# Performance work log

Hardware: AMD Instinct MI355X
Metric: run time of the kernel (lower is better)

## Reference

```python
import jax, jax.numpy as jnp
import numpy as np

# 5x5 Gaussian-Laplacian template: kernel = (4*GL) * GL_T, with a2=-a1/8, a3=-a1/16
GL_T = np.zeros((5, 5), np.float32)
GL_T[2, 2] = 1.0
for r, c in [(1, 2), (2, 1), (2, 3), (3, 2)]:
    GL_T[r, c] = -1.0 / 8.0
for r, c in [(0, 2), (1, 1), (1, 3), (2, 0), (2, 4), (3, 1), (3, 3), (4, 2)]:
    GL_T[r, c] = -1.0 / 16.0

SOB0 = np.array([[1, 2, 1], [0, 0, 0], [-1, -2, -1]], np.float32)
SOB45 = np.array([[2, 1, 0], [1, 0, -1], [0, -1, -2]], np.float32)
SOB90 = np.array([[1, 0, -1], [2, 0, -2], [1, 0, -1]], np.float32)
SOB135 = np.array([[0, -1, -2], [1, 0, -1], [2, 1, 0]], np.float32)

# cubic-spaced threshold value table: (10-0)*(i/100)^3, i=0..100
X_VALUES = np.array([10.0 * (i / 100.0) ** 3 for i in range(101)], np.float32)


def conv2d(x, w, stride=1, padding=0):
    return jax.lax.conv_general_dilated(
        x, w, (stride, stride), ((padding, padding), (padding, padding)),
        dimension_numbers=("NCHW", "OIHW", "NCHW"))


def avg_pool(x, k, s, p):
    # PyTorch AvgPool2d default count_include_pad=True -> divide by k*k always
    s_ = jax.lax.reduce_window(x, 0.0, jax.lax.add, (1, 1, k, k), (1, 1, s, s),
                               ((0, 0), (0, 0), (p, p), (p, p)))
    return s_ / float(k * k)


def _gdm(x, gdm_weight, conv_w, bn_gamma, bn_beta, bn_mean, bn_var):
    x = avg_pool(x, 3, 2, 1)                                  # [B,3,H/2,W/2]
    image_a = jnp.mean(x, axis=1, keepdims=True)              # [B,1,h,w]
    y = conv2d(x, conv_w, stride=2, padding=3)                # ConvBN(3,5,7,s2)
    y = (y - bn_mean[None, :, None, None]) * jax.lax.rsqrt(bn_var + 1e-5)[None, :, None, None]
    y = y * bn_gamma[None, :, None, None] + bn_beta[None, :, None, None]
    weight_att = jnp.tanh(jnp.mean(y, axis=(2, 3)))           # [B,5]

    a1 = gdm_weight[0, 0] * 4.0
    kgl = (a1 * jnp.asarray(GL_T))[None, None]                # [1,1,5,5]
    x_GL = jnp.abs(conv2d(image_a, kgl, stride=1, padding=2))
    x_GL = jnp.where(x_GL < 1e-6, 0.0, x_GL)                  # abs/threshold; relu is no-op

    b, _, h, w = x_GL.shape
    x_t = x_GL.reshape(b, 1, -1)                              # [B,1,HW]
    x_max = jnp.max(x_t, axis=-1)                             # [B,1]
    pos = x_t > 0
    all_sum = jnp.sum(pos, axis=-1)                           # [B,1]
    xv = jnp.asarray(X_VALUES)[None, :, None]                 # [1,101,1]
    sub_sum = jnp.sum(pos & (x_t <= xv), axis=-1)             # [B,101]
    percentage = sub_sum / all_sum                            # [B,101] float

    params = jnp.stack([0.2 + 0.05 * weight_att[:, 1],
                        0.4 + 0.05 * weight_att[:, 2],
                        0.6 + 0.05 * weight_att[:, 3],
                        0.8 + 0.05 * weight_att[:, 4]])       # [4,B]
    thr_pct = jnp.sort(params, axis=0).T                      # [B,4]
    z = jnp.abs(percentage[:, None, :] - thr_pct[:, :, None]) # [B,4,101]
    closest = jnp.argmin(z, axis=-1)                          # [B,4]
    threshold = jnp.asarray(X_VALUES)[closest]                # [B,4]

    tmin = jnp.concatenate([jnp.zeros_like(x_max), threshold], axis=-1)[:, :, None]  # [B,5,1]
    tmax = jnp.concatenate([threshold, x_max], axis=-1)[:, :, None]                  # [B,5,1]
    mask = ((x_t > tmin) & (x_t <= tmax)).astype(jnp.float32)                        # [B,5,HW]
    m = mask.reshape(b, 5, h, w)

    m = avg_pool(m, 9, 1, 4)
    m = avg_pool(m, 9, 1, 4)
    m = avg_pool(m, 9, 2, 4)                                  # [B,5,h/2,w/2]
    mf = m.reshape(b, 5, -1)
    mn = jnp.min(mf, axis=2, keepdims=True)
    mx = jnp.max(mf, axis=2, keepdims=True)
    return ((mf - mn) / (mx - mn)).reshape(b, 5, h // 2, w // 2)


def _hge(feat, hge_weight, fc_w, fc_b):
    # directional kernels built from entries of the learned 3x3 weight
    Sob0 = hge_weight[:, :, 0, 0][:, :, None, None]
    Sob45 = hge_weight[:, :, 0, 1][:, :, None, None]
    Sob90 = hge_weight[:, :, 0, 2][:, :, None, None]
    Sob135 = hge_weight[:, :, 1, 0][:, :, None, None]
    a1 = (hge_weight[:, :, 2, 2] * 4.0)[:, :, None, None]
    x_0 = conv2d(feat, Sob0 * jnp.asarray(SOB0), 1, 1)
    x_45 = conv2d(feat, Sob45 * jnp.asarray(SOB45), 1, 1)
    x_90 = conv2d(feat, Sob90 * jnp.asarray(SOB90), 1, 1)
    x_135 = conv2d(feat, Sob135 * jnp.asarray(SOB135), 1, 1)
    x_GL = conv2d(feat, a1 * jnp.asarray(GL_T), 1, 2)
    x_out = jnp.concatenate([x_0, x_45, x_90, x_135, x_GL], axis=1)  # [B,5*C,H,W]
    return conv2d(x_out, fc_w) + fc_b[None, :, None, None]


def setup_inputs() -> dict:
    key = jax.random.key(0)
    ks = jax.random.split(key, 6)
    return {
        "x": jax.random.normal(ks[0], (8, 3, 512, 512), jnp.float32),
        "gdm_weight": jax.random.normal(ks[1], (1, 5), jnp.float32) * 0.5,
        "conv_w": jax.random.normal(ks[2], (5, 3, 7, 7), jnp.float32) * 0.05,
        "bn_gamma": jnp.ones((5,), jnp.float32),
        "bn_beta": jnp.zeros((5,), jnp.float32),
        "bn_mean": jnp.zeros((5,), jnp.float32),
        "bn_var": jnp.ones((5,), jnp.float32),
        "feat": jax.random.normal(ks[3], (8, 64, 128, 128), jnp.float32),
        "hge_weight": jax.random.normal(ks[4], (64, 64, 3, 3), jnp.float32) * 0.05,
        "fc_w": jax.random.normal(ks[5], (64, 320, 1, 1), jnp.float32) * 0.05,
        "fc_b": jnp.zeros((64,), jnp.float32),
    }


def reference(x, gdm_weight, conv_w, bn_gamma, bn_beta, bn_mean, bn_var,
              feat, hge_weight, fc_w, fc_b):
    gdm_out = _gdm(x, gdm_weight, conv_w, bn_gamma, bn_beta, bn_mean, bn_var)
    hge_out = _hge(feat, hge_weight, fc_w, fc_b)
    return gdm_out, hge_out
```

## Files before the change

### kernel.cpp

```cpp
#include <hip/hip_runtime.h>
#include <hip/hip_bf16.h>
#include <math.h>

#define WS_AT    0
#define WS_YSUM  20480
#define WS_XMAX  20520
#define WS_HIST  20528
#define WS_MN    21376
#define WS_MX    21440
#define WS_XP    21504
#define WS_IA    1594368
#define WS_XGL   2118656

#define GDM_OUT  655360

static __device__ __forceinline__ float xv_val(int i) {
    double t = (double)i / 100.0;
    return (float)(10.0 * t * t * t);
}

__global__ __launch_bounds__(256) void k_front(const float* __restrict__ x,
                                               const float* __restrict__ hw,
                                               const float* __restrict__ fcw,
                                               float* __restrict__ xp,
                                               float* __restrict__ ia,
                                               float* __restrict__ At,
                                               float* __restrict__ zr,
                                               unsigned* __restrict__ mnb,
                                               unsigned* __restrict__ mxb) {
    int bid = blockIdx.x;
    if (bid < 2048) {
        int idx = bid * 256 + threadIdx.x;
        int b = idx >> 16; int p = idx & 65535; int oy = p >> 8; int ox = p & 255;
        float cs[3];
#pragma unroll
        for (int c = 0; c < 3; ++c) {
            const float* src = x + (((size_t)(b * 3 + c)) << 18);
            float s = 0.f;
#pragma unroll
            for (int dy = -1; dy <= 1; ++dy) {
                int iy = 2 * oy + dy; if ((unsigned)iy >= 512u) continue;
#pragma unroll
                for (int dx = -1; dx <= 1; ++dx) {
                    int ix = 2 * ox + dx; if ((unsigned)ix >= 512u) continue;
                    s += src[iy * 512 + ix];
                }
            }
            cs[c] = s * (1.f / 9.f);
            xp[(((size_t)(b * 3 + c)) << 16) + p] = cs[c];
        }
        ia[(((size_t)b) << 16) + p] = (cs[0] + cs[1] + cs[2]) * (1.f / 3.f);
    } else if (bid < 2128) {
        int idx = (bid - 2048) * 256 + threadIdx.x;
        int o = idx & 63; int k = idx >> 6;
        int d = k >> 6; int c = k & 63;
        const int goff[5] = {0, 1, 2, 3, 8};
        float s = 0.f;
        for (int m = 0; m < 64; ++m)
            s += fcw[o * 320 + d * 64 + m] * hw[(m * 64 + c) * 9 + goff[d]];
        At[k * 64 + o] = s * ((d == 4) ? 4.f : 1.f);
    } else {
#pragma unroll
        for (int q = 0; q < 4; ++q) {
            int i = threadIdx.x + 256 * q;
            if (i < 864) zr[i] = 0.f;
        }
        if (threadIdx.x < 40) mnb[threadIdx.x] = 0x7f7fffffu;
        else if (threadIdx.x < 80) mxb[threadIdx.x - 40] = 0u;
    }
}

__global__ __launch_bounds__(256) void k_convgl(const float* __restrict__ xp,
                                                const float* __restrict__ w,
                                                float* __restrict__ ysum,
                                                const float* __restrict__ ia,
                                                const float* __restrict__ gdmw,
                                                float* __restrict__ xgl,
                                                int* __restrict__ hist,
                                                unsigned* __restrict__ xmax) {
    __shared__ float wsm[735];
    __shared__ float red[256];
    __shared__ float xv[101];
    __shared__ int sh[102];
    int bid = blockIdx.x;
    int tid = threadIdx.x;
    if (bid < 512) {
        int b = bid >> 6;
        int p = (bid & 63) * 256 + tid;
        int oy = p >> 7, ox = p & 127;
        for (int l = tid; l < 735; l += 256) wsm[l] = w[l];
        __syncthreads();
        float s[5] = {0.f, 0.f, 0.f, 0.f, 0.f};
        for (int ic = 0; ic < 3; ++ic) {
            const float* src = xp + (((size_t)(b * 3 + ic)) << 16);
#pragma unroll
            for (int r = 0; r < 7; ++r) {
                int iy = 2 * oy - 3 + r; if ((unsigned)iy >= 256u) continue;
#pragma unroll
                for (int ss = 0; ss < 7; ++ss) {
                    int ix = 2 * ox - 3 + ss; if ((unsigned)ix >= 256u) continue;
                    float v = src[iy * 256 + ix];
                    int wi = (ic * 7 + r) * 7 + ss;
#pragma unroll
                    for (int co = 0; co < 5; ++co) s[co] = fmaf(wsm[co * 147 + wi], v, s[co]);
                }
            }
        }
#pragma unroll
        for (int co = 0; co < 5; ++co) {
            red[tid] = s[co]; __syncthreads();
            for (int off = 128; off > 0; off >>= 1) {
                if (tid < off) red[tid] += red[tid + off];
                __syncthreads();
            }
            if (tid == 0) atomicAdd(&ysum[b * 5 + co], red[0]);
            __syncthreads();
        }
    } else {
        int idx = bid - 512;
        int b = idx >> 8;
        int p = (idx & 255) * 256 + tid;
        int y = p >> 8, x = p & 255;
        if (tid < 101) xv[tid] = xv_val(tid);
        if (tid < 102) sh[tid] = 0;
        __syncthreads();
        const float* src = ia + (((size_t)b) << 16);
        float a1 = gdmw[0] * 4.f;
        auto rd = [&](int dy, int dx) -> float {
            int iy = y + dy, ix = x + dx;
            if ((unsigned)iy >= 256u || (unsigned)ix >= 256u) return 0.f;
            return src[iy * 256 + ix];
        };
        float acc = rd(0, 0)
            - 0.125f  * (rd(-1, 0) + rd(0, -1) + rd(0, 1) + rd(1, 0))
            - 0.0625f * (rd(-2, 0) + rd(-1, -1) + rd(-1, 1) + rd(0, -2) +
                         rd(0, 2) + rd(1, -1) + rd(1, 1) + rd(2, 0));
        float raw = fabsf(a1 * acc);
        float val = (raw < 1e-6f) ? 0.f : raw;
        xgl[(((size_t)b) << 16) + p] = val;
        if (val > 0.f) {
            int lo = 0, hi = 101;
            while (lo < hi) { int mid = (lo + hi) >> 1; if (val <= xv[mid]) hi = mid; else lo = mid + 1; }
            atomicAdd(&sh[lo], 1);
        }
        red[tid] = val; __syncthreads();
        for (int off = 128; off > 0; off >>= 1) {
            if (tid < off) red[tid] = fmaxf(red[tid], red[tid + off]);
            __syncthreads();
        }
        if (tid == 0) atomicMax(&xmax[b], __float_as_uint(red[0]));
        if (tid < 102 && sh[tid]) atomicAdd(&hist[b * 102 + tid], sh[tid]);
    }
}

#define F1_STR 268
__global__ __launch_bounds__(256) void k_hv1(const float* __restrict__ in,
                                             const float* __restrict__ ysum,
                                             const float* __restrict__ gamma,
                                             const float* __restrict__ beta,
                                             const float* __restrict__ mean,
                                             const float* __restrict__ var,
                                             const int* __restrict__ hist,
                                             const unsigned* __restrict__ xmax,
                                             float* __restrict__ outp) {
    int plane = blockIdx.y;
    int r0 = blockIdx.x * 8;
    int b = plane / 5, band = plane - 5 * b;
    __shared__ float sthr[4];
    int tid = threadIdx.x;
    if (tid == 0) {
        float wa[5];
        for (int c = 1; c < 5; ++c) {
            float m = ysum[b * 5 + c] * (1.f / 16384.f);
            wa[c] = tanhf((m - mean[c]) * rsqrtf(var[c] + 1e-5f) * gamma[c] + beta[c]);
        }
        float pr[4] = {0.2f + 0.05f * wa[1], 0.4f + 0.05f * wa[2],
                       0.6f + 0.05f * wa[3], 0.8f + 0.05f * wa[4]};
        auto sw = [&](int i, int j) { if (pr[i] > pr[j]) { float t = pr[i]; pr[i] = pr[j]; pr[j] = t; } };
        sw(0, 1); sw(2, 3); sw(0, 2); sw(1, 3); sw(1, 2);
        int all = 0;
        for (int i = 0; i <= 101; ++i) all += hist[b * 102 + i];
        float bestz[4] = {1e30f, 1e30f, 1e30f, 1e30f};
        int besti[4] = {0, 0, 0, 0};
        int cum = 0;
        for (int i = 0; i <= 100; ++i) {
            cum += hist[b * 102 + i];
            float pct = (float)cum / (float)all;
            for (int t = 0; t < 4; ++t) {
                float z = fabsf(pct - pr[t]);
                if (z < bestz[t]) { bestz[t] = z; besti[t] = i; }
            }
        }
        for (int t = 0; t < 4; ++t) sthr[t] = xv_val(besti[t]);
    }
    __syncthreads();
    float tmin = (band == 0) ? 0.f : sthr[band - 1];
    float tmax = (band == 4) ? __uint_as_float(xmax[b]) : sthr[band];
    const float* src = in + (((size_t)b) << 16);
    __shared__ float mr[16][F1_STR];
    __shared__ float hh[16][256];
    for (int l = tid; l < 16 * 256; l += 256) {
        int i = l >> 8, c = l & 255;
        int rr = r0 - 4 + i;
        float v = ((unsigned)rr < 256u) ? src[rr * 256 + c] : 0.f;
        v = (v > tmin && v <= tmax) ? 1.f : 0.f;
        mr[i][c + 4] = v;
    }
    if (tid < 128) { int i = tid >> 3, p = tid & 7; mr[i][p < 4 ? p : 256 + p] = 0.f; }
    __syncthreads();
    {
        int r = tid >> 4, x0 = (tid & 15) * 16;
        float w[24];
#pragma unroll
        for (int k = 0; k < 6; ++k) {
            float4 q = *(const float4*)&mr[r][x0 + 4 * k];
            w[4 * k] = q.x; w[4 * k + 1] = q.y; w[4 * k + 2] = q.z; w[4 * k + 3] = q.w;
        }
        float o[16];
        float s = 0.f;
#pragma unroll
        for (int k = 0; k < 9; ++k) s += w[k];
#pragma unroll
        for (int j = 0; j < 16; ++j) {
            o[j] = s * (1.f / 9.f);
            if (j < 15) s += w[j + 9] - w[j];
        }
#pragma unroll
        for (int k = 0; k < 4; ++k) {
            float4 q = {o[4 * k], o[4 * k + 1], o[4 * k + 2], o[4 * k + 3]};
            *(float4*)&hh[r][x0 + 4 * k] = q;
        }
    }
    __syncthreads();
    {
        int c = tid;
        float ld[16];
#pragma unroll
        for (int i = 0; i < 16; ++i) ld[i] = hh[i][c];
        float s = 0.f;
#pragma unroll
        for (int k = 0; k < 9; ++k) s += ld[k];
        float* dst = outp + (((size_t)plane) << 16);
#pragma unroll
        for (int j = 0; j < 8; ++j) {
            dst[(r0 + j) * 256 + c] = s * (1.f / 9.f);
            if (j < 7) s += ld[j + 9] - ld[j];
        }
    }
}

__global__ __launch_bounds__(256) void k_hv2s2(const float* __restrict__ in,
                                               float* __restrict__ outp,
                                               unsigned* __restrict__ mnb,
                                               unsigned* __restrict__ mxb) {
    int plane = blockIdx.y;
    int r0 = blockIdx.x * 8;
    __shared__ float mr[31][264];
    __shared__ float hh[31][256];
    int tid = threadIdx.x;
    const float* src = in + (((size_t)plane) << 16);
    for (int l = tid; l < 31 * 264; l += 256) {
        int i = l / 264, c = l - i * 264;
        int rr = 2 * r0 - 8 + i, cc = c - 4;
        mr[i][c] = ((unsigned)rr < 256u && (unsigned)cc < 256u) ? src[rr * 256 + cc] : 0.f;
    }
    __syncthreads();
    for (int l = tid; l < 31 * 256; l += 256) {
        int i = l >> 8, x = l & 255;
        float s = 0.f;
#pragma unroll
        for (int k = 0; k < 9; ++k) s += mr[i][x + k];
        hh[i][x] = s * (1.f / 9.f);
    }
    __syncthreads();
    for (int l = tid; l < 23 * 256; l += 256) {
        int i2 = l >> 8, x = l & 255;
        float s = 0.f;
#pragma unroll
        for (int k = 0; k < 9; ++k) s += hh[i2 + k][x];
        float v = s * (1.f / 9.f);
        if ((unsigned)(2 * r0 - 4 + i2) >= 256u) v = 0.f;
        mr[i2][x + 4] = v;
    }
    if (tid < 184) { int i2 = tid / 8, p = tid & 7; mr[i2][p < 4 ? p : 256 + p] = 0.f; }
    __syncthreads();
    for (int l = tid; l < 23 * 128; l += 256) {
        int i2 = l >> 7, ox = l & 127;
        float s = 0.f;
#pragma unroll
        for (int k = 0; k < 9; ++k) s += mr[i2][2 * ox + k];
        hh[i2][ox] = s * (1.f / 9.f);
    }
    __syncthreads();
    float vmn = 1e30f, vmx = -1e30f;
    float* dst = outp + (size_t)plane * 16384;
#pragma unroll
    for (int q = 0; q < 4; ++q) {
        int l = tid + 256 * q;
        int jj = l >> 7, ox = l & 127;
        float s = 0.f;
#pragma unroll
        for (int k = 0; k < 9; ++k) s += hh[2 * jj + k][ox];
        s *= (1.f / 9.f);
        dst[(r0 + jj) * 128 + ox] = s;
        vmn = fminf(vmn, s); vmx = fmaxf(vmx, s);
    }
    __syncthreads();
    float* smn = &hh[23][0];
    float* smx = &hh[24][0];
    smn[tid] = vmn; smx[tid] = vmx; __syncthreads();
    for (int off = 128; off > 0; off >>= 1) {
        if (tid < off) {
            smn[tid] = fminf(smn[tid], smn[tid + off]);
            smx[tid] = fmaxf(smx[tid], smx[tid + off]);
        }
        __syncthreads();
    }
    if (tid == 0) {
        atomicMin(&mnb[plane], __float_as_uint(smn[0]));
        atomicMax(&mxb[plane], __float_as_uint(smx[0]));
    }
}

__global__ __launch_bounds__(512, 2) void k_hge(const float* __restrict__ feat,
                                                const float* __restrict__ At,
                                                const float* __restrict__ fcb,
                                                const float* __restrict__ p2,
                                                const unsigned* __restrict__ mnb,
                                                const unsigned* __restrict__ mxb,
                                                float* __restrict__ gdm,
                                                float* __restrict__ out) {
    int tile = blockIdx.x, b = blockIdx.y;
    int tid = threadIdx.x;
    if (tile == 64) {
        int base = b * 512 + tid;
#pragma unroll
        for (int q = 0; q < 40; ++q) {
            int i4 = base + 4096 * q;
            int idx = i4 * 4;
            int plane = idx >> 14;
            float mn = __uint_as_float(mnb[plane]), mx = __uint_as_float(mxb[plane]);
            float inv = 1.f / (mx - mn);
            float4 v = *(const float4*)&p2[idx];
            float4 o = {(v.x - mn) * inv, (v.y - mn) * inv, (v.z - mn) * inv, (v.w - mn) * inv};
            *(float4*)&gdm[idx] = o;
        }
        return;
    }
    int ty = (tile >> 3) * 16, tx = (tile & 7) * 16;
    int grp = tid >> 8, tg = tid & 255;
    __shared__ float ft[2][20][21];
    __shared__ float tl[2][5][256];
    __shared__ float al[2][2][5][64];
    int og = tg >> 6;
    int pl = tg & 63;
    float acc[4][8];
#pragma unroll
    for (int i = 0; i < 4; ++i)
#pragma unroll
        for (int j = 0; j < 8; ++j) acc[i][j] = 0.f;

    const float* cur[3];
    int str3[3];
    bool ok[3];
#pragma unroll
    for (int j = 0; j < 3; ++j) {
        int l = tid + 512 * j;
        cur[j] = nullptr; str3[j] = 0; ok[j] = false;
        if (l < 800) {
            int ch = (l >= 400); int rem = l - ch * 400;
            int r = rem / 20, cx = rem - r * 20;
            int gy = ty - 2 + r, gx = tx - 2 + cx;
            if ((unsigned)gy < 128u && (unsigned)gx < 128u) {
                cur[j] = feat + (((size_t)(b * 64 + ch)) << 14) + gy * 128 + gx;
                str3[j] = 2 << 14;
                ok[j] = true;
            }
        } else if (l < 1440) {
            int q = l - 800;
            int ch = (q >= 320); int k = q - ch * 320;
            cur[j] = At + (k >> 6) * 4096 + ch * 64 + (k & 63);
            str3[j] = 128;
            ok[j] = true;
        }
    }
    float pr[3];
#pragma unroll
    for (int j = 0; j < 3; ++j) pr[j] = ok[j] ? *cur[j] : 0.f;

    for (int g = 0; g < 32; ++g) {
        int buf = g & 1;
#pragma unroll
        for (int j = 0; j < 3; ++j) {
            int l = tid + 512 * j;
            if (l < 800) {
                int ch = (l >= 400); int rem = l - ch * 400;
                int r = rem / 20, cx = rem - r * 20;
                ft[ch][r][cx] = pr[j];
            } else if (l < 1440) {
                ((float*)al[buf])[l - 800] = pr[j];
            }
        }
        __syncthreads();
        if (g < 31) {
#pragma unroll
            for (int j = 0; j < 3; ++j) {
                if (ok[j]) { cur[j] += str3[j]; pr[j] = *cur[j]; }
            }
        }
        {
            int cy = (tg >> 4) + 2, cx = (tg & 15) + 2;
            int ch = grp;
            float fm2 = ft[ch][cy - 2][cx], f2p = ft[ch][cy + 2][cx];
            float fl2 = ft[ch][cy][cx - 2], fr2 = ft[ch][cy][cx + 2];
            float a  = ft[ch][cy - 1][cx - 1], bq = ft[ch][cy - 1][cx], cc = ft[ch][cy - 1][cx + 1];
            float dd = ft[ch][cy][cx - 1],     ee = ft[ch][cy][cx],     ffv = ft[ch][cy][cx + 1];
            float g_ = ft[ch][cy + 1][cx - 1], h  = ft[ch][cy + 1][cx], i2 = ft[ch][cy + 1][cx + 1];
            tl[ch][0][tg] = (a + 2.f * bq + cc) - (g_ + 2.f * h + i2);
            tl[ch][1][tg] = 2.f * a + bq + dd - ffv - h - 2.f * i2;
            tl[ch][2][tg] = (a - cc) + 2.f * (dd - ffv) + (g_ - i2);
            tl[ch][3][tg] = -bq - 2.f * cc + dd - ffv + 2.f * g_ + h;
            tl[ch][4][tg] = ee - 0.125f * (bq + dd + ffv + h)
                          - 0.0625f * (fm2 + a + cc + fl2 + fr2 + g_ + i2 + f2p);
        }
        __syncthreads();
#pragma unroll
        for (int ch = 0; ch < 2; ++ch) {
#pragma unroll
            for (int d = 0; d < 5; ++d) {
                float4 a0 = *(const float4*)&al[buf][ch][d][grp * 32 + og * 8];
                float4 a1 = *(const float4*)&al[buf][ch][d][grp * 32 + og * 8 + 4];
                float av[8] = {a0.x, a0.y, a0.z, a0.w, a1.x, a1.y, a1.z, a1.w};
#pragma unroll
                for (int pj = 0; pj < 4; ++pj) {
                    float tv = tl[ch][d][pl + 64 * pj];
#pragma unroll
                    for (int oi = 0; oi < 8; ++oi)
                        acc[pj][oi] = fmaf(av[oi], tv, acc[pj][oi]);
                }
            }
        }
    }
#pragma unroll
    for (int oi = 0; oi < 8; ++oi) {
        int o = grp * 32 + og * 8 + oi;
        float bias = fcb[o];
        float* dsto = out + (((size_t)(b * 64 + o)) << 14);
#pragma unroll
        for (int pj = 0; pj < 4; ++pj) {
            int pxl = pl + 64 * pj;
            dsto[(ty + (pxl >> 4)) * 128 + tx + (pxl & 15)] = acc[pj][oi] + bias;
        }
    }
}

extern "C" void kernel_launch(void* const* d_in, const int* in_sizes, int n_in,
                              void* d_out, int out_size, void* d_ws, size_t ws_size,
                              hipStream_t stream) {
    const float* x    = (const float*)d_in[0];
    const float* gdmw = (const float*)d_in[1];
    const float* convw= (const float*)d_in[2];
    const float* bng  = (const float*)d_in[3];
    const float* bnb  = (const float*)d_in[4];
    const float* bnm  = (const float*)d_in[5];
    const float* bnv  = (const float*)d_in[6];
    const float* feat = (const float*)d_in[7];
    const float* hw   = (const float*)d_in[8];
    const float* fcw  = (const float*)d_in[9];
    const float* fcb  = (const float*)d_in[10];
    float* out = (float*)d_out;
    float* ws  = (float*)d_ws;

    float* At   = ws + WS_AT;
    float* ysum = ws + WS_YSUM;
    unsigned* xmax = (unsigned*)(ws + WS_XMAX);
    int* hist   = (int*)(ws + WS_HIST);
    unsigned* mnb = (unsigned*)(ws + WS_MN);
    unsigned* mxb = (unsigned*)(ws + WS_MX);
    float* xp   = ws + WS_XP;
    float* ia   = ws + WS_IA;
    float* xgl  = ws + WS_XGL;
    float* p2   = ws + WS_XP + 20480;

    float* hge = out + GDM_OUT;
    float* p0  = hge;

    k_front  <<<2129, 256, 0, stream>>>(x, hw, fcw, xp, ia, At, ws + WS_YSUM, mnb, mxb);
    k_convgl <<<2560, 256, 0, stream>>>(xp, convw, ysum, ia, gdmw, xgl, hist, xmax);
    k_hv1    <<<dim3(32, 40), 256, 0, stream>>>(xgl, ysum, bng, bnb, bnm, bnv, hist, xmax, p0);
    k_hv2s2  <<<dim3(16, 40), 256, 0, stream>>>(p0, p2, mnb, mxb);
    k_hge    <<<dim3(65, 8), 512, 0, stream>>>(feat, At, fcb, p2, mnb, mxb, out, hge);
}
```

Before: 251.5 us.

## Fuse band-mask box filter and stride-2 pooling into one kernel

Merges the first 9x9 box filter over the thresholded band mask with the second 9x9 filter and the stride-2 pooling into a single kernel. The intermediate full-resolution plane no longer goes through global memory, and one launch is removed. In exchange each block recomputes a larger halo (39 mask rows), does more shared-memory work, and uses about 74KB of LDS, which may lower occupancy.

```diff
diff --git a/kernel.cpp b/kernel.cpp
--- a/kernel.cpp
+++ b/kernel.cpp
@@ -153,19 +153,22 @@
     }
 }
 
-#define F1_STR 268
-__global__ __launch_bounds__(256) void k_hv1(const float* __restrict__ in,
-                                             const float* __restrict__ ysum,
-                                             const float* __restrict__ gamma,
-                                             const float* __restrict__ beta,
-                                             const float* __restrict__ mean,
-                                             const float* __restrict__ var,
-                                             const int* __restrict__ hist,
-                                             const unsigned* __restrict__ xmax,
-                                             float* __restrict__ outp) {
+__global__ __launch_bounds__(256) void k_pool(const float* __restrict__ xgl,
+                                              const float* __restrict__ ysum,
+                                              const float* __restrict__ gamma,
+                                              const float* __restrict__ beta,
+                                              const float* __restrict__ mean,
+                                              const float* __restrict__ var,
+                                              const int* __restrict__ hist,
+                                              const unsigned* __restrict__ xmax,
+                                              float* __restrict__ p2,
+                                              unsigned* __restrict__ mnb,
+                                              unsigned* __restrict__ mxb) {
     int plane = blockIdx.y;
     int r0 = blockIdx.x * 8;
     int b = plane / 5, band = plane - 5 * b;
+    __shared__ float mk[39][264];
+    __shared__ float p1[31][264];
     __shared__ float sthr[4];
     int tid = threadIdx.x;
     if (tid == 0) {
@@ -174,9 +177,9 @@
             float m = ysum[b * 5 + c] * (1.f / 16384.f);
             wa[c] = tanhf((m - mean[c]) * rsqrtf(var[c] + 1e-5f) * gamma[c] + beta[c]);
         }
-        float pr[4] = {0.2f + 0.05f * wa[1], 0.4f + 0.05f * wa[2],
-                       0.6f + 0.05f * wa[3], 0.8f + 0.05f * wa[4]};
-        auto sw = [&](int i, int j) { if (pr[i] > pr[j]) { float t = pr[i]; pr[i] = pr[j]; pr[j] = t; } };
+        float pr_[4] = {0.2f + 0.05f * wa[1], 0.4f + 0.05f * wa[2],
+                        0.6f + 0.05f * wa[3], 0.8f + 0.05f * wa[4]};
+        auto sw = [&](int i, int j) { if (pr_[i] > pr_[j]) { float t = pr_[i]; pr_[i] = pr_[j]; pr_[j] = t; } };
         sw(0, 1); sw(2, 3); sw(0, 2); sw(1, 3); sw(1, 2);
         int all = 0;
         for (int i = 0; i <= 101; ++i) all += hist[b * 102 + i];
@@ -187,7 +190,7 @@
             cum += hist[b * 102 + i];
             float pct = (float)cum / (float)all;
             for (int t = 0; t < 4; ++t) {
-                float z = fabsf(pct - pr[t]);
+                float z = fabsf(pct - pr_[t]);
                 if (z < bestz[t]) { bestz[t] = z; besti[t] = i; }
             }
         }
@@ -196,118 +199,90 @@
     __syncthreads();
     float tmin = (band == 0) ? 0.f : sthr[band - 1];
     float tmax = (band == 4) ? __uint_as_float(xmax[b]) : sthr[band];
-    const float* src = in + (((size_t)b) << 16);
-    __shared__ float mr[16][F1_STR];
-    __shared__ float hh[16][256];
-    for (int l = tid; l < 16 * 256; l += 256) {
-        int i = l >> 8, c = l & 255;
-        int rr = r0 - 4 + i;
-        float v = ((unsigned)rr < 256u) ? src[rr * 256 + c] : 0.f;
-        v = (v > tmin && v <= tmax) ? 1.f : 0.f;
-        mr[i][c + 4] = v;
-    }
-    if (tid < 128) { int i = tid >> 3, p = tid & 7; mr[i][p < 4 ? p : 256 + p] = 0.f; }
-    __syncthreads();
-    {
-        int r = tid >> 4, x0 = (tid & 15) * 16;
-        float w[24];
-#pragma unroll
-        for (int k = 0; k < 6; ++k) {
-            float4 q = *(const float4*)&mr[r][x0 + 4 * k];
-            w[4 * k] = q.x; w[4 * k + 1] = q.y; w[4 * k + 2] = q.z; w[4 * k + 3] = q.w;
-        }
-        float o[16];
-        float s = 0.f;
-#pragma unroll
-        for (int k = 0; k < 9; ++k) s += w[k];
-#pragma unroll
-        for (int j = 0; j < 16; ++j) {
-            o[j] = s * (1.f / 9.f);
-            if (j < 15) s += w[j + 9] - w[j];
-        }
-#pragma unroll
-        for (int k = 0; k < 4; ++k) {
-            float4 q = {o[4 * k], o[4 * k + 1], o[4 * k + 2], o[4 * k + 3]};
-            *(float4*)&hh[r][x0 + 4 * k] = q;
-        }
+    const float* src = xgl + (((size_t)b) << 16);
+    for (int l = tid; l < 39 * 264; l += 256) {
+        int i = l / 264, c = l - i * 264;
+        int rr = 2 * r0 - 12 + i, cc = c - 4;
+        float m = 0.f;
+        if ((unsigned)rr < 256u && (unsigned)cc < 256u) {
+            float v = src[rr * 256 + cc];
+            m = (v > tmin && v <= tmax) ? 1.f : 0.f;
+        }
+        mk[i][c] = m;
     }
     __syncthreads();
     {
         int c = tid;
-        float ld[16];
-#pragma unroll
-        for (int i = 0; i < 16; ++i) ld[i] = hh[i][c];
-        float s = 0.f;
-#pragma unroll
-        for (int k = 0; k < 9; ++k) s += ld[k];
-        float* dst = outp + (((size_t)plane) << 16);
-#pragma unroll
-        for (int j = 0; j < 8; ++j) {
-            dst[(r0 + j) * 256 + c] = s * (1.f / 9.f);
-            if (j < 7) s += ld[j + 9] - ld[j];
-        }
-    }
-}
-
-__global__ __launch_bounds__(256) void k_hv2s2(const float* __restrict__ in,
-                                               float* __restrict__ outp,
-                                               unsigned* __restrict__ mnb,
-                                               unsigned* __restrict__ mxb) {
-    int plane = blockIdx.y;
-    int r0 = blockIdx.x * 8;
-    __shared__ float mr[31][264];
-    __shared__ float hh[31][256];
-    int tid = threadIdx.x;
-    const float* src = in + (((size_t)plane) << 16);
-    for (int l = tid; l < 31 * 264; l += 256) {
-        int i = l / 264, c = l - i * 264;
-        int rr = 2 * r0 - 8 + i, cc = c - 4;
-        mr[i][c] = ((unsigned)rr < 256u && (unsigned)cc < 256u) ? src[rr * 256 + cc] : 0.f;
-    }
-    __syncthreads();
-    for (int l = tid; l < 31 * 256; l += 256) {
-        int i = l >> 8, x = l & 255;
-        float s = 0.f;
-#pragma unroll
-        for (int k = 0; k < 9; ++k) s += mr[i][x + k];
-        hh[i][x] = s * (1.f / 9.f);
-    }
-    __syncthreads();
-    for (int l = tid; l < 23 * 256; l += 256) {
-        int i2 = l >> 8, x = l & 255;
-        float s = 0.f;
-#pragma unroll
-        for (int k = 0; k < 9; ++k) s += hh[i2 + k][x];
-        float v = s * (1.f / 9.f);
-        if ((unsigned)(2 * r0 - 4 + i2) >= 256u) v = 0.f;
-        mr[i2][x + 4] = v;
-    }
-    if (tid < 184) { int i2 = tid / 8, p = tid & 7; mr[i2][p < 4 ? p : 256 + p] = 0.f; }
+        auto hb = [&](int q) -> float {
+            float s = 0.f;
+#pragma unroll
+            for (int k = 0; k < 9; ++k) s += mk[q][c + k];
+            return s;
+        };
+        float w9[9]; float rs = 0.f;
+#pragma unroll
+        for (int q = 0; q < 8; ++q) { float h = hb(q); w9[q] = h; rs += h; }
+#pragma unroll
+        for (int pr = 0; pr < 31; ++pr) {
+            int q = pr + 8;
+            float h = hb(q); w9[q % 9] = h; rs += h;
+            float val = rs * (1.f / 81.f);
+            int ar = 2 * r0 - 8 + pr;
+            if ((unsigned)ar >= 256u) val = 0.f;
+            p1[pr][c + 4] = val;
+            rs -= w9[pr % 9];
+        }
+    }
+    if (tid < 248) { int i = tid >> 3, p = tid & 7; p1[i][p < 4 ? p : 256 + p] = 0.f; }
+    __syncthreads();
+    {
+        int c = tid;
+        auto hb2 = [&](int q) -> float {
+            float s = 0.f;
+#pragma unroll
+            for (int k = 0; k < 9; ++k) s += p1[q][c + k];
+            return s;
+        };
+        float w9[9]; float rs = 0.f;
+#pragma unroll
+        for (int q = 0; q < 8; ++q) { float h = hb2(q); w9[q] = h; rs += h; }
+#pragma unroll
+        for (int i2 = 0; i2 < 23; ++i2) {
+            int q = i2 + 8;
+            float h = hb2(q); w9[q % 9] = h; rs += h;
+            float val = rs * (1.f / 81.f);
+            int ar = 2 * r0 - 4 + i2;
+            if ((unsigned)ar >= 256u) val = 0.f;
+            mk[i2][c + 4] = val;
+            rs -= w9[i2 % 9];
+        }
+    }
+    if (tid < 184) { int i2 = tid >> 3, p = tid & 7; mk[i2][p < 4 ? p : 256 + p] = 0.f; }
     __syncthreads();
     for (int l = tid; l < 23 * 128; l += 256) {
         int i2 = l >> 7, ox = l & 127;
         float s = 0.f;
 #pragma unroll
-        for (int k = 0; k < 9; ++k) s += mr[i2][2 * ox + k];
-        hh[i2][ox] = s * (1.f / 9.f);
+        for (int k = 0; k < 9; ++k) s += mk[i2][2 * ox + k];
+        p1[i2][ox] = s * (1.f / 9.f);
     }
     __syncthreads();
     float vmn = 1e30f, vmx = -1e30f;
-    float* dst = outp + (size_t)plane * 16384;
+    float* dst = p2 + (size_t)plane * 16384;
 #pragma unroll
     for (int q = 0; q < 4; ++q) {
         int l = tid + 256 * q;
         int jj = l >> 7, ox = l & 127;
         float s = 0.f;
 #pragma unroll
-        for (int k = 0; k < 9; ++k) s += hh[2 * jj + k][ox];
+        for (int k = 0; k < 9; ++k) s += p1[2 * jj + k][ox];
         s *= (1.f / 9.f);
         dst[(r0 + jj) * 128 + ox] = s;
         vmn = fminf(vmn, s); vmx = fmaxf(vmx, s);
     }
     __syncthreads();
-    float* smn = &hh[23][0];
-    float* smx = &hh[24][0];
+    float* smn = &mk[0][0];
+    float* smx = &mk[1][0];
     smn[tid] = vmn; smx[tid] = vmx; __syncthreads();
     for (int off = 128; off > 0; off >>= 1) {
         if (tid < off) {
@@ -483,11 +458,10 @@
     float* p2   = ws + WS_XP + 20480;
 
     float* hge = out + GDM_OUT;
-    float* p0  = hge;
 
     k_front  <<<2129, 256, 0, stream>>>(x, hw, fcw, xp, ia, At, ws + WS_YSUM, mnb, mxb);
     k_convgl <<<2560, 256, 0, stream>>>(xp, convw, ysum, ia, gdmw, xgl, hist, xmax);
-    k_hv1    <<<dim3(32, 40), 256, 0, stream>>>(xgl, ysum, bng, bnb, bnm, bnv, hist, xmax, p0);
-    k_hv2s2  <<<dim3(16, 40), 256, 0, stream>>>(p0, p2, mnb, mxb);
+    k_pool   <<<dim3(16, 40), 256, 0, stream>>>(xgl, ysum, bng, bnb, bnm, bnv, hist, xmax,
+                                                p2, mnb, mxb);
     k_hge    <<<dim3(65, 8), 512, 0, stream>>>(feat, At, fcb, p2, mnb, mxb, out, hge);
 }
```

New measurement: 242.1 us. -3.8%, faster.
